# Performance work log

Hardware: AMD Instinct MI355X
Metric: run time of the kernel (lower is better)

## Reference

```python
import jax, jax.numpy as jnp
import numpy as np

EMBED_DIM = 128
N_CLASSES = 5
NX = 1024
NY = 1024


def setup_inputs() -> dict:
    key = jax.random.key(0)
    k1, k2 = jax.random.split(key)
    z_x = jax.random.normal(k1, (NX, EMBED_DIM), dtype=jnp.float32)
    z_y = jax.random.normal(k2, (NY, EMBED_DIM), dtype=jnp.float32)
    # Parameter init exactly as in __init__ for the L1 compare
    ex = 2 * np.sqrt(2 / np.pi) * EMBED_DIM
    var = 4 * (1 - 2 / np.pi) * EMBED_DIM
    beta_init = ex / np.sqrt(var)
    theta = jnp.ones((1, N_CLASSES - 1), dtype=jnp.float32) / np.sqrt(var)  # clamped >=0, already positive
    beta = jnp.full((N_CLASSES - 1,), beta_init, dtype=jnp.float32)
    return {"z_x": z_x, "z_y": z_y, "theta": theta, "beta": beta}


def reference(z_x, z_y, theta, beta):
    # L1 compare: s[i,j] = -sum_d |z_x[i,d] - z_y[j,d]|   -> (Nx, Ny)
    s = -jnp.sum(jnp.abs(z_x[:, None, :] - z_y[None, :, :]), axis=-1)
    # SSA: dual softmax soft alignment
    a = jax.nn.softmax(s, axis=1)  # row softmax
    b = jax.nn.softmax(s, axis=0)  # column softmax
    a = a + b - a * b
    a = a / jnp.sum(a)
    # weighted reduction -> scalar similarity
    c = jnp.sum(a * s)
    logits = c * theta + beta  # (1, n_classes-1) broadcast
    return logits.reshape(-1)
```

## Files before the change

kernel.cpp:

```cpp
#include <hip/hip_runtime.h>
#include <math.h>

#define NXC 1024
#define NYC 1024
#define DC  128
#define NCM1 4
#define NTILE 256

#define WS_ROWP  0
#define WS_COLP  65536
#define WS_PART  131072

typedef _Float16 half2v __attribute__((ext_vector_type(2)));
union H2U { half2v h; unsigned u; };
union F2U { float2 f; unsigned long long u; };

#if defined(__has_builtin)
#if __has_builtin(__builtin_amdgcn_fdot2)
#define HAVE_FDOT2 1
#endif
#endif

__device__ unsigned g_rowdone[16 * 16];
__device__ unsigned g_coldone[16 * 16];
__device__ unsigned g_done = 0;

__device__ __forceinline__ void st_agent_f2(float* p, float2 v) {
    F2U u; u.f = v;
    __hip_atomic_store((unsigned long long*)p, u.u, __ATOMIC_RELAXED,
                       __HIP_MEMORY_SCOPE_AGENT);
}
__device__ __forceinline__ float2 ld_agent_f2(const float* p) {
    F2U u;
    u.u = __hip_atomic_load((const unsigned long long*)p, __ATOMIC_RELAXED,
                            __HIP_MEMORY_SCOPE_AGENT);
    return u.f;
}
__device__ __forceinline__ unsigned ld_agent_u32(const unsigned* p) {
    return __hip_atomic_load(p, __ATOMIC_RELAXED, __HIP_MEMORY_SCOPE_AGENT);
}

__device__ __forceinline__ float absdiff_dot(uint4 xa, uint4 ya, float acc)
{
    const unsigned* xu = (const unsigned*)&xa;
    const unsigned* yu = (const unsigned*)&ya;
    half2v one; one.x = (_Float16)1.f; one.y = (_Float16)1.f;
    #pragma unroll
    for (int q = 0; q < 4; ++q) {
        H2U x, y, d;
        x.u = xu[q]; y.u = yu[q];
        d.h = x.h - y.h;
        d.u &= 0x7FFF7FFFu;
#ifdef HAVE_FDOT2
        acc = __builtin_amdgcn_fdot2(d.h, one, acc, false);
#else
        acc += (float)d.h.x + (float)d.h.y;
#endif
    }
    return acc;
}

__global__ __launch_bounds__(512, 1) void ssa_fused_kernel(
    const float* __restrict__ zx, const float* __restrict__ zy,
    const float* __restrict__ theta, const float* __restrict__ beta,
    float* __restrict__ ws, float* __restrict__ out)
{
    __shared__ __align__(16) _Float16 xs[64 * 128];
    __shared__ __align__(16) _Float16 ys[64 * 128];
    __shared__ float cpm[32][65], cpl[32][65];
    __shared__ float rm_s[64], rl_s[64], cm_s[64], cl_s[64];
    __shared__ float red0[8], red1[8];
    __shared__ unsigned last_flag;

    float* rowp = ws + WS_ROWP;
    float* colp = ws + WS_COLP;
    float* part = ws + WS_PART;

    const int t    = threadIdx.x;
    const int tile = blockIdx.x;
    const int bx   = tile & 15;
    const int by   = tile >> 4;
    const int x0   = by * 64;
    const int y0   = bx * 64;

    #pragma unroll
    for (int k = 0; k < 2; ++k) {
        int idx = t + k * 512;
        int r   = idx >> 4;
        int j   = idx & 15;
        int off = r * 128 + 8 * (j ^ ((r >> 2) & 7));
        const float4* gx = (const float4*)(zx + (size_t)(x0 + r) * DC + 8 * j);
        float4 v0 = gx[0], v1 = gx[1];
        uint4 hx;
        {
            H2U a, b, c, d;
            a.h.x = (_Float16)v0.x; a.h.y = (_Float16)v0.y;
            b.h.x = (_Float16)v0.z; b.h.y = (_Float16)v0.w;
            c.h.x = (_Float16)v1.x; c.h.y = (_Float16)v1.y;
            d.h.x = (_Float16)v1.z; d.h.y = (_Float16)v1.w;
            hx.x = a.u; hx.y = b.u; hx.z = c.u; hx.w = d.u;
        }
        *(uint4*)(xs + off) = hx;
    }
    #pragma unroll
    for (int k = 0; k < 2; ++k) {
        int idx = t + k * 512;
        int r   = idx >> 4;
        int j   = idx & 15;
        int off = r * 128 + 8 * (j ^ ((r >> 2) & 7));
        const float4* gy = (const float4*)(zy + (size_t)(y0 + r) * DC + 8 * j);
        float4 v0 = gy[0], v1 = gy[1];
        uint4 hy;
        {
            H2U a, b, c, d;
            a.h.x = (_Float16)v0.x; a.h.y = (_Float16)v0.y;
            b.h.x = (_Float16)v0.z; b.h.y = (_Float16)v0.w;
            c.h.x = (_Float16)v1.x; c.h.y = (_Float16)v1.y;
            d.h.x = (_Float16)v1.z; d.h.y = (_Float16)v1.w;
            hy.x = a.u; hy.y = b.u; hy.z = c.u; hy.w = d.u;
        }
        *(uint4*)(ys + off) = hy;
    }
    __syncthreads();

    const int tx = t & 15;
    const int ty = t >> 4;
    const int xswz = (ty >> 1) & 7;
    const int yswz = tx & 7;

    const _Float16* xb = xs + (2 * ty) * 128;
    const _Float16* yb = ys + (4 * tx) * 128;

    float acc[2][4];
    #pragma unroll
    for (int i = 0; i < 2; ++i)
        #pragma unroll
        for (int j = 0; j < 4; ++j) acc[i][j] = 0.f;

    uint4 xc0 = *(const uint4*)(xb +       8 * (0 ^ xswz));
    uint4 xc1 = *(const uint4*)(xb + 128 + 8 * (0 ^ xswz));
    uint4 yc0 = *(const uint4*)(yb +       8 * (0 ^ yswz));
    uint4 yc1 = *(const uint4*)(yb + 128 + 8 * (0 ^ yswz));
    uint4 yc2 = *(const uint4*)(yb + 256 + 8 * (0 ^ yswz));
    uint4 yc3 = *(const uint4*)(yb + 384 + 8 * (0 ^ yswz));

    #pragma unroll 4
    for (int j = 0; j < 16; ++j) {
        uint4 xa0 = xc0, xa1 = xc1, ya0 = yc0, ya1 = yc1, ya2 = yc2, ya3 = yc3;
        const int jn = (j + 1) & 15;
        xc0 = *(const uint4*)(xb +       8 * (jn ^ xswz));
        xc1 = *(const uint4*)(xb + 128 + 8 * (jn ^ xswz));
        yc0 = *(const uint4*)(yb +       8 * (jn ^ yswz));
        yc1 = *(const uint4*)(yb + 128 + 8 * (jn ^ yswz));
        yc2 = *(const uint4*)(yb + 256 + 8 * (jn ^ yswz));
        yc3 = *(const uint4*)(yb + 384 + 8 * (jn ^ yswz));

        acc[0][0] = absdiff_dot(xa0, ya0, acc[0][0]);
        acc[0][1] = absdiff_dot(xa0, ya1, acc[0][1]);
        acc[0][2] = absdiff_dot(xa0, ya2, acc[0][2]);
        acc[0][3] = absdiff_dot(xa0, ya3, acc[0][3]);
        acc[1][0] = absdiff_dot(xa1, ya0, acc[1][0]);
        acc[1][1] = absdiff_dot(xa1, ya1, acc[1][1]);
        acc[1][2] = absdiff_dot(xa1, ya2, acc[1][2]);
        acc[1][3] = absdiff_dot(xa1, ya3, acc[1][3]);
    }

    float sv[2][4];
    #pragma unroll
    for (int i = 0; i < 2; ++i)
        #pragma unroll
        for (int j = 0; j < 4; ++j) sv[i][j] = -acc[i][j];

    #pragma unroll
    for (int i = 0; i < 2; ++i) {
        float m = fmaxf(fmaxf(sv[i][0], sv[i][1]), fmaxf(sv[i][2], sv[i][3]));
        float l = __expf(sv[i][0] - m) + __expf(sv[i][1] - m)
                + __expf(sv[i][2] - m) + __expf(sv[i][3] - m);
        #pragma unroll
        for (int off = 1; off < 16; off <<= 1) {
            float mo = __shfl_xor(m, off, 64);
            float lo = __shfl_xor(l, off, 64);
            float nm = fmaxf(m, mo);
            l = l * __expf(m - nm) + lo * __expf(mo - nm);
            m = nm;
        }
        if (tx == 0)
            st_agent_f2(rowp + 2 * ((size_t)(x0 + 2 * ty + i) * 16 + bx),
                        make_float2(m, l));
    }

    #pragma unroll
    for (int j = 0; j < 4; ++j) {
        float m = fmaxf(sv[0][j], sv[1][j]);
        float l = __expf(sv[0][j] - m) + __expf(sv[1][j] - m);
        cpm[ty][4 * tx + j] = m;
        cpl[ty][4 * tx + j] = l;
    }
    __syncthreads();
    if (t < 64) {
        float m = cpm[0][t], l = cpl[0][t];
        #pragma unroll 8
        for (int k = 1; k < 32; ++k) {
            float mo = cpm[k][t], lo = cpl[k][t];
            float nm = fmaxf(m, mo);
            l = l * __expf(m - nm) + lo * __expf(mo - nm);
            m = nm;
        }
        st_agent_f2(colp + 2 * ((size_t)(y0 + t) * 16 + by), make_float2(m, l));
    }

    __syncthreads();
    if (t == 0) {
        __hip_atomic_fetch_add(&g_rowdone[by * 16], 1u, __ATOMIC_RELAXED,
                               __HIP_MEMORY_SCOPE_AGENT);
        __hip_atomic_fetch_add(&g_coldone[bx * 16], 1u, __ATOMIC_RELAXED,
                               __HIP_MEMORY_SCOPE_AGENT);
        while (ld_agent_u32(&g_rowdone[by * 16]) < 16u)
            __builtin_amdgcn_s_sleep(8);
        while (ld_agent_u32(&g_coldone[bx * 16]) < 16u)
            __builtin_amdgcn_s_sleep(8);
    }
    __syncthreads();

    const int item  = t >> 3;
    const int lane8 = t & 7;
    {
        float2 e0 = ld_agent_f2(rowp + 2 * ((size_t)(x0 + item) * 16 + 2 * lane8));
        float2 e1 = ld_agent_f2(rowp + 2 * ((size_t)(x0 + item) * 16 + 2 * lane8 + 1));
        float m = fmaxf(e0.x, e1.x);
        float l = e0.y * __expf(e0.x - m) + e1.y * __expf(e1.x - m);
        #pragma unroll
        for (int off = 1; off < 8; off <<= 1) {
            float mo = __shfl_xor(m, off, 64);
            float lo = __shfl_xor(l, off, 64);
            float nm = fmaxf(m, mo);
            l = l * __expf(m - nm) + lo * __expf(mo - nm);
            m = nm;
        }
        if (lane8 == 0) { rm_s[item] = m; rl_s[item] = 1.f / l; }
    }
    {
        float2 e0 = ld_agent_f2(colp + 2 * ((size_t)(y0 + item) * 16 + 2 * lane8));
        float2 e1 = ld_agent_f2(colp + 2 * ((size_t)(y0 + item) * 16 + 2 * lane8 + 1));
        float m = fmaxf(e0.x, e1.x);
        float l = e0.y * __expf(e0.x - m) + e1.y * __expf(e1.x - m);
        #pragma unroll
        for (int off = 1; off < 8; off <<= 1) {
            float mo = __shfl_xor(m, off, 64);
            float lo = __shfl_xor(l, off, 64);
            float nm = fmaxf(m, mo);
            l = l * __expf(m - nm) + lo * __expf(mo - nm);
            m = nm;
        }
        if (lane8 == 0) { cm_s[item] = m; cl_s[item] = 1.f / l; }
    }
    __syncthreads();

    float S0 = 0.f, S1 = 0.f;
    #pragma unroll
    for (int i = 0; i < 2; ++i) {
        const float rm = rm_s[2 * ty + i];
        const float rl = rl_s[2 * ty + i];
        #pragma unroll
        for (int j = 0; j < 4; ++j) {
            const float cm = cm_s[4 * tx + j];
            const float cl = cl_s[4 * tx + j];
            float s = sv[i][j];
            float a = __expf(s - rm) * rl;
            float b = __expf(s - cm) * cl;
            float w = a + b - a * b;
            S0 += w;
            S1 += w * s;
        }
    }
    #pragma unroll
    for (int off = 32; off; off >>= 1) {
        S0 += __shfl_xor(S0, off, 64);
        S1 += __shfl_xor(S1, off, 64);
    }
    if ((t & 63) == 0) { red0[t >> 6] = S0; red1[t >> 6] = S1; }
    __syncthreads();
    if (t == 0) {
        float t0 = 0.f, t1 = 0.f;
        #pragma unroll
        for (int w = 0; w < 8; ++w) { t0 += red0[w]; t1 += red1[w]; }
        st_agent_f2(part + 2 * tile, make_float2(t0, t1));
    }

    __syncthreads();
    if (t == 0) {
        unsigned prev = __hip_atomic_fetch_add(&g_done, 1u, __ATOMIC_RELAXED,
                                               __HIP_MEMORY_SCOPE_AGENT);
        last_flag = (prev == NTILE - 1u) ? 1u : 0u;
    }
    __syncthreads();

    if (last_flag) {
        float P0 = 0.f, P1 = 0.f;
        if (t < NTILE) {
            float2 p = ld_agent_f2(part + 2 * t);
            P0 = p.x; P1 = p.y;
        }
        #pragma unroll
        for (int off = 32; off; off >>= 1) {
            P0 += __shfl_xor(P0, off, 64);
            P1 += __shfl_xor(P1, off, 64);
        }
        if ((t & 63) == 0) { red0[t >> 6] = P0; red1[t >> 6] = P1; }
        if (t < 16) {
            __hip_atomic_store(&g_rowdone[t * 16], 0u, __ATOMIC_RELAXED,
                               __HIP_MEMORY_SCOPE_AGENT);
            __hip_atomic_store(&g_coldone[t * 16], 0u, __ATOMIC_RELAXED,
                               __HIP_MEMORY_SCOPE_AGENT);
        }
        if (t == 16)
            __hip_atomic_store(&g_done, 0u, __ATOMIC_RELAXED,
                               __HIP_MEMORY_SCOPE_AGENT);
        __syncthreads();
        if (t < NCM1) {
            float t0 = 0.f, t1 = 0.f;
            #pragma unroll
            for (int w = 0; w < 8; ++w) { t0 += red0[w]; t1 += red1[w]; }
            float c = t1 / t0;
            out[t] = c * theta[t] + beta[t];
        }
    }
}

extern "C" void kernel_launch(void* const* d_in, const int* in_sizes, int n_in,
                              void* d_out, int out_size, void* d_ws, size_t ws_size,
                              hipStream_t stream)
{
    const float* zx    = (const float*)d_in[0];
    const float* zy    = (const float*)d_in[1];
    const float* theta = (const float*)d_in[2];
    const float* beta  = (const float*)d_in[3];
    float* out = (float*)d_out;
    float* ws  = (float*)d_ws;

    ssa_fused_kernel<<<NTILE, 512, 0, stream>>>(zx, zy, theta, beta, ws, out);
}
```

Measured before the change: 75.37 us.

## Split each 64x64 tile into two 256-thread blocks of 64x32

Doubles the grid to 512 blocks of 256 threads, each computing a 64x32 tile, so more blocks can be resident per CU and more CUs are busy. Row partials grow to 32 per row, column partials shrink to 16, and the partial reads switch from agent-scoped atomic loads to plain float4 vector loads. The spin waits now depend on 32 blocks per row group, sleep for shorter intervals, and the X tile load is repeated in both halves. Plain loads after the relaxed barrier could in principle read stale data.

After: 77.75 us. 1.03x slower.

```diff
diff --git a/kernel.cpp b/kernel.cpp
--- a/kernel.cpp
+++ b/kernel.cpp
@@ -5,11 +5,11 @@
 #define NYC 1024
 #define DC  128
 #define NCM1 4
-#define NTILE 256
-
-#define WS_ROWP  0
-#define WS_COLP  65536
-#define WS_PART  131072
+#define NBLK 512
+
+#define WS_ROWP 0
+#define WS_COLP 65536
+#define WS_PART 98304
 
 typedef _Float16 half2v __attribute__((ext_vector_type(2)));
 union H2U { half2v h; unsigned u; };
@@ -22,19 +22,13 @@
 #endif
 
 __device__ unsigned g_rowdone[16 * 16];
-__device__ unsigned g_coldone[16 * 16];
+__device__ unsigned g_coldone[32 * 16];
 __device__ unsigned g_done = 0;
 
 __device__ __forceinline__ void st_agent_f2(float* p, float2 v) {
     F2U u; u.f = v;
     __hip_atomic_store((unsigned long long*)p, u.u, __ATOMIC_RELAXED,
                        __HIP_MEMORY_SCOPE_AGENT);
-}
-__device__ __forceinline__ float2 ld_agent_f2(const float* p) {
-    F2U u;
-    u.u = __hip_atomic_load((const unsigned long long*)p, __ATOMIC_RELAXED,
-                            __HIP_MEMORY_SCOPE_AGENT);
-    return u.f;
 }
 __device__ __forceinline__ unsigned ld_agent_u32(const unsigned* p) {
     return __hip_atomic_load(p, __ATOMIC_RELAXED, __HIP_MEMORY_SCOPE_AGENT);
@@ -60,16 +54,16 @@
     return acc;
 }
 
-__global__ __launch_bounds__(512, 1) void ssa_fused_kernel(
+__global__ __launch_bounds__(256, 2) void ssa_fused_kernel(
     const float* __restrict__ zx, const float* __restrict__ zy,
     const float* __restrict__ theta, const float* __restrict__ beta,
     float* __restrict__ ws, float* __restrict__ out)
 {
     __shared__ __align__(16) _Float16 xs[64 * 128];
-    __shared__ __align__(16) _Float16 ys[64 * 128];
-    __shared__ float cpm[32][65], cpl[32][65];
-    __shared__ float rm_s[64], rl_s[64], cm_s[64], cl_s[64];
-    __shared__ float red0[8], red1[8];
+    __shared__ __align__(16) _Float16 ys[32 * 128];
+    __shared__ float cpm[32][32], cpl[32][32];
+    __shared__ float rm_s[64], rl_s[64], cm_s[32], cl_s[32];
+    __shared__ float red0[4], red1[4];
     __shared__ unsigned last_flag;
 
     float* rowp = ws + WS_ROWP;
@@ -77,15 +71,16 @@
     float* part = ws + WS_PART;
 
     const int t    = threadIdx.x;
-    const int tile = blockIdx.x;
+    const int tile = blockIdx.x >> 1;
+    const int h    = blockIdx.x & 1;
     const int bx   = tile & 15;
     const int by   = tile >> 4;
     const int x0   = by * 64;
-    const int y0   = bx * 64;
-
-    #pragma unroll
-    for (int k = 0; k < 2; ++k) {
-        int idx = t + k * 512;
+    const int y0   = bx * 64 + h * 32;
+
+    #pragma unroll
+    for (int k = 0; k < 4; ++k) {
+        int idx = t + k * 256;
         int r   = idx >> 4;
         int j   = idx & 15;
         int off = r * 128 + 8 * (j ^ ((r >> 2) & 7));
@@ -104,7 +99,7 @@
     }
     #pragma unroll
     for (int k = 0; k < 2; ++k) {
-        int idx = t + k * 512;
+        int idx = t + k * 256;
         int r   = idx >> 4;
         int j   = idx & 15;
         int off = r * 128 + 8 * (j ^ ((r >> 2) & 7));
@@ -123,10 +118,10 @@
     }
     __syncthreads();
 
-    const int tx = t & 15;
-    const int ty = t >> 4;
+    const int tx = t & 7;
+    const int ty = t >> 3;
     const int xswz = (ty >> 1) & 7;
-    const int yswz = tx & 7;
+    const int yswz = tx;
 
     const _Float16* xb = xs + (2 * ty) * 128;
     const _Float16* yb = ys + (4 * tx) * 128;
@@ -177,7 +172,7 @@
         float l = __expf(sv[i][0] - m) + __expf(sv[i][1] - m)
                 + __expf(sv[i][2] - m) + __expf(sv[i][3] - m);
         #pragma unroll
-        for (int off = 1; off < 16; off <<= 1) {
+        for (int off = 1; off < 8; off <<= 1) {
             float mo = __shfl_xor(m, off, 64);
             float lo = __shfl_xor(l, off, 64);
             float nm = fmaxf(m, mo);
@@ -185,7 +180,7 @@
             m = nm;
         }
         if (tx == 0)
-            st_agent_f2(rowp + 2 * ((size_t)(x0 + 2 * ty + i) * 16 + bx),
+            st_agent_f2(rowp + 2 * ((size_t)(x0 + 2 * ty + i) * 32 + bx * 2 + h),
                         make_float2(m, l));
     }
 
@@ -197,7 +192,7 @@
         cpl[ty][4 * tx + j] = l;
     }
     __syncthreads();
-    if (t < 64) {
+    if (t < 32) {
         float m = cpm[0][t], l = cpl[0][t];
         #pragma unroll 8
         for (int k = 1; k < 32; ++k) {
@@ -213,22 +208,46 @@
     if (t == 0) {
         __hip_atomic_fetch_add(&g_rowdone[by * 16], 1u, __ATOMIC_RELAXED,
                                __HIP_MEMORY_SCOPE_AGENT);
-        __hip_atomic_fetch_add(&g_coldone[bx * 16], 1u, __ATOMIC_RELAXED,
-                               __HIP_MEMORY_SCOPE_AGENT);
-        while (ld_agent_u32(&g_rowdone[by * 16]) < 16u)
-            __builtin_amdgcn_s_sleep(8);
-        while (ld_agent_u32(&g_coldone[bx * 16]) < 16u)
-            __builtin_amdgcn_s_sleep(8);
-    }
-    __syncthreads();
-
-    const int item  = t >> 3;
-    const int lane8 = t & 7;
+        __hip_atomic_fetch_add(&g_coldone[(bx * 2 + h) * 16], 1u,
+                               __ATOMIC_RELAXED, __HIP_MEMORY_SCOPE_AGENT);
+        while (ld_agent_u32(&g_rowdone[by * 16]) < 32u)
+            __builtin_amdgcn_s_sleep(2);
+        while (ld_agent_u32(&g_coldone[(bx * 2 + h) * 16]) < 16u)
+            __builtin_amdgcn_s_sleep(2);
+    }
+    __syncthreads();
+
     {
-        float2 e0 = ld_agent_f2(rowp + 2 * ((size_t)(x0 + item) * 16 + 2 * lane8));
-        float2 e1 = ld_agent_f2(rowp + 2 * ((size_t)(x0 + item) * 16 + 2 * lane8 + 1));
-        float m = fmaxf(e0.x, e1.x);
-        float l = e0.y * __expf(e0.x - m) + e1.y * __expf(e1.x - m);
+        const int row   = t >> 2;
+        const int lane4 = t & 3;
+        const float4* rowp4 = (const float4*)rowp;
+        float m = -1e30f, l = 0.f;
+        #pragma unroll
+        for (int k = 0; k < 4; ++k) {
+            float4 q = rowp4[(size_t)(x0 + row) * 16 + 4 * lane4 + k];
+            float mq = fmaxf(q.x, q.z);
+            float lq = q.y * __expf(q.x - mq) + q.w * __expf(q.z - mq);
+            float nm = fmaxf(m, mq);
+            l = l * __expf(m - nm) + lq * __expf(mq - nm);
+            m = nm;
+        }
+        #pragma unroll
+        for (int off = 1; off < 4; off <<= 1) {
+            float mo = __shfl_xor(m, off, 64);
+            float lo = __shfl_xor(l, off, 64);
+            float nm = fmaxf(m, mo);
+            l = l * __expf(m - nm) + lo * __expf(mo - nm);
+            m = nm;
+        }
+        if (lane4 == 0) { rm_s[row] = m; rl_s[row] = 1.f / l; }
+    }
+    {
+        const int col   = t >> 3;
+        const int lane8 = t & 7;
+        const float4* colp4 = (const float4*)colp;
+        float4 q = colp4[(size_t)(y0 + col) * 8 + lane8];
+        float m = fmaxf(q.x, q.z);
+        float l = q.y * __expf(q.x - m) + q.w * __expf(q.z - m);
         #pragma unroll
         for (int off = 1; off < 8; off <<= 1) {
             float mo = __shfl_xor(m, off, 64);
@@ -237,22 +256,7 @@
             l = l * __expf(m - nm) + lo * __expf(mo - nm);
             m = nm;
         }
-        if (lane8 == 0) { rm_s[item] = m; rl_s[item] = 1.f / l; }
-    }
-    {
-        float2 e0 = ld_agent_f2(colp + 2 * ((size_t)(y0 + item) * 16 + 2 * lane8));
-        float2 e1 = ld_agent_f2(colp + 2 * ((size_t)(y0 + item) * 16 + 2 * lane8 + 1));
-        float m = fmaxf(e0.x, e1.x);
-        float l = e0.y * __expf(e0.x - m) + e1.y * __expf(e1.x - m);
-        #pragma unroll
-        for (int off = 1; off < 8; off <<= 1) {
-            float mo = __shfl_xor(m, off, 64);
-            float lo = __shfl_xor(l, off, 64);
-            float nm = fmaxf(m, mo);
-            l = l * __expf(m - nm) + lo * __expf(mo - nm);
-            m = nm;
-        }
-        if (lane8 == 0) { cm_s[item] = m; cl_s[item] = 1.f / l; }
+        if (lane8 == 0) { cm_s[col] = m; cl_s[col] = 1.f / l; }
     }
     __syncthreads();
 
@@ -281,46 +285,42 @@
     if ((t & 63) == 0) { red0[t >> 6] = S0; red1[t >> 6] = S1; }
     __syncthreads();
     if (t == 0) {
-        float t0 = 0.f, t1 = 0.f;
-        #pragma unroll
-        for (int w = 0; w < 8; ++w) { t0 += red0[w]; t1 += red1[w]; }
-        st_agent_f2(part + 2 * tile, make_float2(t0, t1));
+        float t0 = red0[0] + red0[1] + red0[2] + red0[3];
+        float t1 = red1[0] + red1[1] + red1[2] + red1[3];
+        st_agent_f2(part + 2 * blockIdx.x, make_float2(t0, t1));
     }
 
     __syncthreads();
     if (t == 0) {
         unsigned prev = __hip_atomic_fetch_add(&g_done, 1u, __ATOMIC_RELAXED,
                                                __HIP_MEMORY_SCOPE_AGENT);
-        last_flag = (prev == NTILE - 1u) ? 1u : 0u;
+        last_flag = (prev == NBLK - 1u) ? 1u : 0u;
     }
     __syncthreads();
 
     if (last_flag) {
-        float P0 = 0.f, P1 = 0.f;
-        if (t < NTILE) {
-            float2 p = ld_agent_f2(part + 2 * t);
-            P0 = p.x; P1 = p.y;
-        }
+        float4 p = ((const float4*)part)[t];
+        float P0 = p.x + p.z;
+        float P1 = p.y + p.w;
         #pragma unroll
         for (int off = 32; off; off >>= 1) {
             P0 += __shfl_xor(P0, off, 64);
             P1 += __shfl_xor(P1, off, 64);
         }
         if ((t & 63) == 0) { red0[t >> 6] = P0; red1[t >> 6] = P1; }
-        if (t < 16) {
+        if (t < 16)
             __hip_atomic_store(&g_rowdone[t * 16], 0u, __ATOMIC_RELAXED,
                                __HIP_MEMORY_SCOPE_AGENT);
-            __hip_atomic_store(&g_coldone[t * 16], 0u, __ATOMIC_RELAXED,
+        if (t >= 32 && t < 64)
+            __hip_atomic_store(&g_coldone[(t - 32) * 16], 0u, __ATOMIC_RELAXED,
                                __HIP_MEMORY_SCOPE_AGENT);
-        }
-        if (t == 16)
+        if (t == 64)
             __hip_atomic_store(&g_done, 0u, __ATOMIC_RELAXED,
                                __HIP_MEMORY_SCOPE_AGENT);
         __syncthreads();
         if (t < NCM1) {
-            float t0 = 0.f, t1 = 0.f;
-            #pragma unroll
-            for (int w = 0; w < 8; ++w) { t0 += red0[w]; t1 += red1[w]; }
+            float t0 = red0[0] + red0[1] + red0[2] + red0[3];
+            float t1 = red1[0] + red1[1] + red1[2] + red1[3];
             float c = t1 / t0;
             out[t] = c * theta[t] + beta[t];
         }
@@ -338,5 +338,5 @@
     float* out = (float*)d_out;
     float* ws  = (float*)d_ws;
 
-    ssa_fused_kernel<<<NTILE, 512, 0, stream>>>(zx, zy, theta, beta, ws, out);
-}
+    ssa_fused_kernel<<<NBLK, 256, 0, stream>>>(zx, zy, theta, beta, ws, out);
+}
```
